# Kernel tuning notes

Hardware: AMD Instinct MI355X
Metric: run time of the kernel (lower is better)

Reference implementation:

```python
import jax, jax.numpy as jnp
import numpy as np

B, S, HID = 2, 2048, 2048
NH, NKV, HD = 16, 4, 128
GROUPS = NH // NKV
CLIP = 8.0
ROPE_THETA = 500000.0
QKV_OUT = HID + 2 * NKV * HD  # 3072
NEG = jnp.finfo(jnp.float32).min


def setup_inputs() -> dict:
    key = jax.random.key(0)
    k1, k2, k3 = jax.random.split(key, 3)
    hidden_states = jax.random.normal(k1, (B, S, HID), dtype=jnp.float32)
    position_ids = jnp.tile(jnp.arange(S, dtype=jnp.int64)[None, :], (B, 1))
    Wqkv = jax.random.normal(k2, (QKV_OUT, HID), dtype=jnp.float32) * (HID ** -0.5)
    Wout = jax.random.normal(k3, (HID, HID), dtype=jnp.float32) * (HID ** -0.5)
    return {"hidden_states": hidden_states, "position_ids": position_ids,
            "Wqkv": Wqkv, "Wout": Wout}


def _rotate_half(x):
    x1, x2 = jnp.split(x, 2, axis=-1)
    return jnp.concatenate((-x2, x1), axis=-1)


def reference(hidden_states, position_ids, Wqkv, Wout):
    b, s, _ = hidden_states.shape
    # fused QKV projection + clamp
    qkv = jnp.einsum('bsh,oh->bso', hidden_states, Wqkv)
    qkv = jnp.clip(qkv, -CLIP, CLIP)
    q, k, v = jnp.split(qkv, [HID, HID + NKV * HD], axis=2)
    q = q.reshape(b, s, NH, HD).transpose(0, 2, 1, 3)   # [b, nh, s, hd]
    k = k.reshape(b, s, NKV, HD).transpose(0, 2, 1, 3)  # [b, nkv, s, hd]
    v = v.reshape(b, s, NKV, HD).transpose(0, 2, 1, 3)
    # rotary embedding
    inv_freq = 1.0 / (ROPE_THETA ** (jnp.arange(0, HD, 2, dtype=jnp.float32) / HD))
    freqs = position_ids.astype(jnp.float32)[:, :, None] * inv_freq[None, None, :]  # [b,s,hd/2]
    emb = jnp.concatenate((freqs, freqs), axis=-1)      # [b, s, hd]
    cos = jnp.cos(emb)[:, None, :, :]                   # [b, 1, s, hd]
    sin = jnp.sin(emb)[:, None, :, :]
    q = q * cos + _rotate_half(q) * sin
    k = k * cos + _rotate_half(k) * sin
    # repeat kv heads (GQA)
    k = jnp.repeat(k, GROUPS, axis=1)  # [b, nh, s, hd]
    v = jnp.repeat(v, GROUPS, axis=1)
    # attention with additive causal mask
    scores = jnp.einsum('bhqd,bhkd->bhqk', q, k) / jnp.sqrt(jnp.float32(HD))
    causal = jnp.where(jnp.tril(jnp.ones((s, s), dtype=bool)), 0.0, NEG)
    scores = scores + causal[None, None, :, :]
    attn = jax.nn.softmax(scores.astype(jnp.float32), axis=-1).astype(q.dtype)
    out = jnp.einsum('bhqk,bhkd->bhqd', attn, v)
    out = out.transpose(0, 2, 1, 3).reshape(b, s, HID)
    return jnp.einsum('bsh,oh->bso', out, Wout)
```

## Files before the change

kernel.cpp:

```cpp
#include <hip/hip_runtime.h>
#include <stdint.h>

#define S_    2048
#define HID_  2048
#define NH_   16
#define NKV_  4
#define HD_   128

using short4x = __attribute__((ext_vector_type(4))) short;
using short8  = __attribute__((ext_vector_type(8))) short;
using floatx4 = __attribute__((ext_vector_type(4))) float;

#define NEGBIG (-3.0e38f)

__device__ __forceinline__ unsigned short f2bf(float x) {
  union { float f; unsigned u; } v; v.f = x;
  unsigned r = v.u + 0x7fffu + ((v.u >> 16) & 1u);
  return (unsigned short)(r >> 16);
}
__device__ __forceinline__ float bf2f(unsigned short b) {
  union { unsigned u; float f; } v; v.u = ((unsigned)b) << 16;
  return v.f;
}
__device__ __forceinline__ void ld_lds16(const void* g, void* l) {
  __builtin_amdgcn_global_load_lds(
      (const __attribute__((address_space(1))) unsigned*)g,
      (__attribute__((address_space(3))) unsigned*)l, 16, 0, 0);
}

__global__ void k_cvt3(const float* __restrict__ s0, unsigned short* __restrict__ d0, int n0,
                       const float* __restrict__ s1, unsigned short* __restrict__ d1, int n1,
                       const float* __restrict__ s2, unsigned short* __restrict__ d2, int n2) {
  int i = blockIdx.x * blockDim.x + threadIdx.x;
  const float* s; unsigned short* d;
  if (i < n0) { s = s0; d = d0; }
  else if (i < n0 + n1) { s = s1; d = d1; i -= n0; }
  else { s = s2; d = d2; i -= n0 + n1; if (i >= n2) return; }
  float4 v = ((const float4*)s)[i];
  union { unsigned short us[4]; uint2 u2; } u;
  u.us[0] = f2bf(v.x); u.us[1] = f2bf(v.y); u.us[2] = f2bf(v.z); u.us[3] = f2bf(v.w);
  ((uint2*)d)[i] = u.u2;
}

__global__ void k_rope2(unsigned short* __restrict__ Qb, unsigned short* __restrict__ Kb,
                        const int* __restrict__ pos, int nQ, float qscale) {
  int idx = blockIdx.x * blockDim.x + threadIdx.x;
  unsigned short* buf; int nh; float oscale;
  if (idx < nQ) { buf = Qb; nh = NH_; oscale = qscale; }
  else { buf = Kb; nh = NKV_; oscale = 1.0f; idx -= nQ; }
  int d = idx & 63;
  int h = (idx >> 6) % nh;
  int m = idx / (unsigned)(nh << 6);
  float p = (float)pos[m];
  float inv = expf(-(float)d * (13.122363377404328f / 64.0f));
  float f = p * inv;
  float cs = cosf(f), sn = sinf(f);
  size_t base = (size_t)m * (nh * HD_) + h * HD_ + d;
  float x1 = bf2f(buf[base]), x2 = bf2f(buf[base + 64]);
  buf[base]      = f2bf((x1 * cs - x2 * sn) * oscale);
  buf[base + 64] = f2bf((x2 * cs + x1 * sn) * oscale);
}

template <int EPI>
__global__ void __launch_bounds__(256)
k_gemm_bt(const unsigned short* __restrict__ A, const unsigned short* __restrict__ Bw,
          unsigned short* __restrict__ Qb, unsigned short* __restrict__ Kb,
          unsigned short* __restrict__ Vt, float* __restrict__ Of) {
  const int K = HID_;
  __shared__ __align__(16) unsigned short As[128 * 32];
  __shared__ __align__(16) unsigned short Bs[128 * 32];
  const int tid  = threadIdx.x;
  const int wave = tid >> 6, lane = tid & 63;
  const int quad = lane >> 4, l15 = lane & 15;
  const int wm = (wave >> 1) * 64, wn = (wave & 1) * 64;
  const int m0 = blockIdx.x * 128, n0 = blockIdx.y * 128;

  floatx4 acc[4][4] = {};

  const int srow = tid >> 2;
  const int scol = (tid & 3) * 8;
  const unsigned short* Ag0 = A  + (size_t)(m0 + srow)      * K + scol;
  const unsigned short* Ag1 = A  + (size_t)(m0 + 64 + srow) * K + scol;
  const unsigned short* Bg0 = Bw + (size_t)(n0 + srow)      * K + scol;
  const unsigned short* Bg1 = Bw + (size_t)(n0 + 64 + srow) * K + scol;
  unsigned short* lA0 = &As[tid * 8];
  unsigned short* lA1 = &As[2048 + tid * 8];
  unsigned short* lB0 = &Bs[tid * 8];
  unsigned short* lB1 = &Bs[2048 + tid * 8];

  for (int k0 = 0; k0 < K; k0 += 32) {
    __syncthreads();
    ld_lds16(Ag0 + k0, lA0);
    ld_lds16(Ag1 + k0, lA1);
    ld_lds16(Bg0 + k0, lB0);
    ld_lds16(Bg1 + k0, lB1);
    __syncthreads();
    short8 a[4], b[4];
#pragma unroll
    for (int i = 0; i < 4; i++) a[i] = *(const short8*)&As[(wm + i * 16 + l15) * 32 + quad * 8];
#pragma unroll
    for (int j = 0; j < 4; j++) b[j] = *(const short8*)&Bs[(wn + j * 16 + l15) * 32 + quad * 8];
#pragma unroll
    for (int i = 0; i < 4; i++)
#pragma unroll
      for (int j = 0; j < 4; j++)
        acc[i][j] = __builtin_amdgcn_mfma_f32_16x16x32_bf16(a[i], b[j], acc[i][j], 0, 0, 0);
  }

#pragma unroll
  for (int i = 0; i < 4; i++) {
#pragma unroll
    for (int j = 0; j < 4; j++) {
      const int col = n0 + wn + j * 16 + l15;
#pragma unroll
      for (int r = 0; r < 4; r++) {
        const int row = m0 + wm + i * 16 + quad * 4 + r;
        float x = acc[i][j][r];
        if (EPI == 0) {
          x = fminf(fmaxf(x, -8.0f), 8.0f);
          if (col < HID_) {
            Qb[(size_t)row * HID_ + col] = f2bf(x);
          } else if (col < HID_ + NKV_ * HD_) {
            Kb[(size_t)row * (NKV_ * HD_) + (col - HID_)] = f2bf(x);
          } else {
            int oo = col - (HID_ + NKV_ * HD_);
            int kvh = oo >> 7, d = oo & 127;
            int bb = row >> 11, ss = row & 2047;
            Vt[((size_t)((bb * NKV_ + kvh) * HD_ + d) << 11) + ss] = f2bf(x);
          }
        } else {
          Of[(size_t)row * HID_ + col] = x;
        }
      }
    }
  }
}

__global__ void __launch_bounds__(256, 2)
k_attn(const unsigned short* __restrict__ Qb, const unsigned short* __restrict__ Kb,
       const unsigned short* __restrict__ Vt, unsigned short* __restrict__ AO) {
  __shared__ __align__(16) unsigned short sm[2][16384];
  __shared__ __align__(16) unsigned short Pl[4][16][80];

  const int tid  = threadIdx.x;
  const int wave = tid >> 6, lane = tid & 63;
  const int quad = lane >> 4, l15 = lane & 15;
  const int tLow  = blockIdx.x;
  const int tHigh = 31 - tLow;
  const int q0L = tLow * 64, q0H = tHigh * 64;
  const int bh = blockIdx.y;
  const int b = bh >> 4, h = bh & 15;
  const int kvh = h >> 2;

  const int srow = tid >> 2;
  const int scol = (tid & 3) * 8;

  {
    const unsigned short* qgL = Qb + (size_t)(b * S_ + q0L + srow) * HID_ + h * HD_ + scol;
    const unsigned short* qgH = Qb + (size_t)(b * S_ + q0H + srow) * HID_ + h * HD_ + scol;
#pragma unroll
    for (int i = 0; i < 4; i++) ld_lds16(qgL + i * 32, &sm[0][i * 2048 + tid * 8]);
#pragma unroll
    for (int i = 0; i < 4; i++) ld_lds16(qgH + i * 32, &sm[1][i * 2048 + tid * 8]);
  }
  __syncthreads();
  short8 qaL[4], qaH[4];
#pragma unroll
  for (int c = 0; c < 4; c++) {
    qaL[c] = *(const short8*)&sm[0][(c * 64 + wave * 16 + l15) * 32 + quad * 8];
    qaH[c] = *(const short8*)&sm[1][(c * 64 + wave * 16 + l15) * 32 + quad * 8];
  }
  __syncthreads();

  floatx4 oacL[8] = {}, oacH[8] = {};
  floatx4 oacEL = {}, oacEH = {};
  float mL = NEGBIG, mH = NEGBIG;

  const unsigned short* kgb = Kb + (size_t)b * S_ * (NKV_ * HD_) + kvh * HD_ + scol;
  const unsigned short* vgb = Vt + (size_t)(b * NKV_ + kvh) * HD_ * S_;

  unsigned short* PlW = &Pl[wave][0][0];

  short8 ones;
#pragma unroll
  for (int i = 0; i < 8; i++) ones[i] = (short)0x3F80;

  auto stage = [&](int bufI, int j) {
    unsigned short* B = &sm[bufI][0];
    const unsigned short* kg = kgb + (size_t)(j * 64 + srow) * (NKV_ * HD_);
#pragma unroll
    for (int i = 0; i < 4; i++) ld_lds16(kg + i * 32, &B[i * 2048 + tid * 8]);
#pragma unroll
    for (int i = 0; i < 4; i++) {
      int c = i >> 1, rowd = (i & 1) * 64 + srow;
      ld_lds16(vgb + (size_t)rowd * S_ + j * 64 + c * 32 + scol,
               &B[8192 + c * 4096 + (i & 1) * 2048 + tid * 8]);
    }
  };

  auto softmax_tile = [&](floatx4* sc, floatx4* oac, floatx4& oacE, float& m_run,
                          int q0, int j, bool diag, short8& pa0, short8& pa1) {
    if (diag) {
      const int rowq = q0 + wave * 16 + l15;
#pragma unroll
      for (int t = 0; t < 4; t++) {
        const int kb0 = j * 64 + t * 16 + quad * 4;
#pragma unroll
        for (int r = 0; r < 4; r++)
          if (kb0 + r > rowq) sc[t][r] = NEGBIG;
      }
    }
    float mx = sc[0][0];
#pragma unroll
    for (int t = 0; t < 4; t++)
#pragma unroll
      for (int r = 0; r < 4; r++) mx = fmaxf(mx, sc[t][r]);
    mx = fmaxf(mx, __shfl_xor(mx, 16));
    mx = fmaxf(mx, __shfl_xor(mx, 32));

    const float mo = m_run;
    m_run = fmaxf(mo, mx);
    if (__any(mx > mo)) {
      float alpha = __builtin_amdgcn_exp2f(mo - m_run);
      float al4[4];
#pragma unroll
      for (int r = 0; r < 4; r++) al4[r] = __shfl(alpha, quad * 4 + r, 16);
#pragma unroll
      for (int t = 0; t < 8; t++)
#pragma unroll
        for (int r = 0; r < 4; r++) oac[t][r] *= al4[r];
#pragma unroll
      for (int r = 0; r < 4; r++) oacE[r] *= al4[r];
    }
#pragma unroll
    for (int t = 0; t < 4; t++) {
      short4x pk;
#pragma unroll
      for (int r = 0; r < 4; r++)
        pk[r] = (short)f2bf(__builtin_amdgcn_exp2f(sc[t][r] - m_run));
      *(short4x*)&PlW[l15 * 80 + t * 16 + quad * 4] = pk;
    }
    pa0 = *(const short8*)&PlW[l15 * 80 + quad * 8];
    pa1 = *(const short8*)&PlW[l15 * 80 + 32 + quad * 8];
  };

  auto step_two = [&](int j, const unsigned short* Kt, const unsigned short* Vts,
                      bool diagL, bool diagH) {
    floatx4 scH[4] = {}, scL[4] = {};
#pragma unroll
    for (int t = 0; t < 4; t++)
#pragma unroll
      for (int c = 0; c < 4; c++) {
        short8 ka = *(const short8*)&Kt[c * 2048 + (t * 16 + l15) * 32 + quad * 8];
        scH[t] = __builtin_amdgcn_mfma_f32_16x16x32_bf16(ka, qaH[c], scH[t], 0, 0, 0);
        scL[t] = __builtin_amdgcn_mfma_f32_16x16x32_bf16(ka, qaL[c], scL[t], 0, 0, 0);
      }
    short8 paH0, paH1, paL0, paL1;
    softmax_tile(scH, oacH, oacEH, mH, q0H, j, diagH, paH0, paH1);
    softmax_tile(scL, oacL, oacEL, mL, q0L, j, diagL, paL0, paL1);
#pragma unroll
    for (int t = 0; t < 8; t++) {
      short8 vb0 = *(const short8*)&Vts[(t * 16 + l15) * 32 + quad * 8];
      oacH[t] = __builtin_amdgcn_mfma_f32_16x16x32_bf16(paH0, vb0, oacH[t], 0, 0, 0);
      oacL[t] = __builtin_amdgcn_mfma_f32_16x16x32_bf16(paL0, vb0, oacL[t], 0, 0, 0);
      short8 vb1 = *(const short8*)&Vts[4096 + (t * 16 + l15) * 32 + quad * 8];
      oacH[t] = __builtin_amdgcn_mfma_f32_16x16x32_bf16(paH1, vb1, oacH[t], 0, 0, 0);
      oacL[t] = __builtin_amdgcn_mfma_f32_16x16x32_bf16(paL1, vb1, oacL[t], 0, 0, 0);
    }
    oacEH = __builtin_amdgcn_mfma_f32_16x16x32_bf16(paH0, ones, oacEH, 0, 0, 0);
    oacEH = __builtin_amdgcn_mfma_f32_16x16x32_bf16(paH1, ones, oacEH, 0, 0, 0);
    oacEL = __builtin_amdgcn_mfma_f32_16x16x32_bf16(paL0, ones, oacEL, 0, 0, 0);
    oacEL = __builtin_amdgcn_mfma_f32_16x16x32_bf16(paL1, ones, oacEL, 0, 0, 0);
  };

  auto step_one = [&](int j, const unsigned short* Kt, const unsigned short* Vts, bool diagH) {
    floatx4 scH[4] = {};
#pragma unroll
    for (int t = 0; t < 4; t++)
#pragma unroll
      for (int c = 0; c < 4; c++) {
        short8 ka = *(const short8*)&Kt[c * 2048 + (t * 16 + l15) * 32 + quad * 8];
        scH[t] = __builtin_amdgcn_mfma_f32_16x16x32_bf16(ka, qaH[c], scH[t], 0, 0, 0);
      }
    short8 paH0, paH1;
    softmax_tile(scH, oacH, oacEH, mH, q0H, j, diagH, paH0, paH1);
#pragma unroll
    for (int t = 0; t < 8; t++) {
      short8 vb0 = *(const short8*)&Vts[(t * 16 + l15) * 32 + quad * 8];
      oacH[t] = __builtin_amdgcn_mfma_f32_16x16x32_bf16(paH0, vb0, oacH[t], 0, 0, 0);
      short8 vb1 = *(const short8*)&Vts[4096 + (t * 16 + l15) * 32 + quad * 8];
      oacH[t] = __builtin_amdgcn_mfma_f32_16x16x32_bf16(paH1, vb1, oacH[t], 0, 0, 0);
    }
    oacEH = __builtin_amdgcn_mfma_f32_16x16x32_bf16(paH0, ones, oacEH, 0, 0, 0);
    oacEH = __builtin_amdgcn_mfma_f32_16x16x32_bf16(paH1, ones, oacEH, 0, 0, 0);
  };

  stage(0, 0);
  int cur = 0;
  for (int j = 0; j <= tHigh; ++j) {
    __syncthreads();
    if (j < tHigh) stage(cur ^ 1, j + 1);
    const unsigned short* Kt  = &sm[cur][0];
    const unsigned short* Vts = Kt + 8192;
    if (j <= tLow) step_two(j, Kt, Vts, j == tLow, j == tHigh);
    else           step_one(j, Kt, Vts, j == tHigh);
    cur ^= 1;
  }

#pragma unroll
  for (int t = 0; t < 8; t++)
#pragma unroll
    for (int r = 0; r < 4; r++) {
      int rgL = q0L + wave * 16 + quad * 4 + r;
      int rgH = q0H + wave * 16 + quad * 4 + r;
      AO[(size_t)(b * S_ + rgL) * HID_ + h * HD_ + t * 16 + l15] = f2bf(oacL[t][r] / oacEL[r]);
      AO[(size_t)(b * S_ + rgH) * HID_ + h * HD_ + t * 16 + l15] = f2bf(oacH[t][r] / oacEH[r]);
    }
}

extern "C" void kernel_launch(void* const* d_in, const int* in_sizes, int n_in,
                              void* d_out, int out_size, void* d_ws, size_t ws_size,
                              hipStream_t stream) {
  (void)in_sizes; (void)n_in; (void)out_size; (void)ws_size;
  const float* hidden = (const float*)d_in[0];
  const int*   pos    = (const int*)d_in[1];
  const float* Wqkv   = (const float*)d_in[2];
  const float* Wout   = (const float*)d_in[3];
  float* out = (float*)d_out;

  unsigned short* ws = (unsigned short*)d_ws;
  const size_t M1 = 1024 * 1024;
  unsigned short* hb  = ws;
  unsigned short* wqb = ws + 8 * M1;
  unsigned short* wob = ws + 14 * M1;
  unsigned short* Qb  = ws + 18 * M1;
  unsigned short* Kb  = ws + 26 * M1;
  unsigned short* Vt  = ws + 28 * M1;
  unsigned short* AO  = hb;

  const float QSCL = 0.08838834764831845f * 1.4426950408889634f;
  const int nQrope = 2 * 2048 * NH_ * 64;
  const int nKrope = 2 * 2048 * NKV_ * 64;

  k_cvt3<<<18432, 256, 0, stream>>>(hidden, hb, 2097152,
                                    Wqkv, wqb, 1572864,
                                    Wout, wob, 1048576);
  k_gemm_bt<0><<<dim3(32, 24), 256, 0, stream>>>(hb, wqb, Qb, Kb, Vt, nullptr);
  k_rope2<<<(nQrope + nKrope) / 256, 256, 0, stream>>>(Qb, Kb, pos, nQrope, QSCL);
  k_attn<<<dim3(16, 32), 256, 0, stream>>>(Qb, Kb, Vt, AO);
  k_gemm_bt<1><<<dim3(32, 16), 256, 0, stream>>>(AO, wob, nullptr, nullptr, nullptr, out);
}
```

Measured before the change: 319.6 us.

## Use hardware bf16 pack, deepen GEMM k-step, and swizzle block order

Replaces software round-to-nearest bf16 conversion with the v_cvt_pk_bf16_f32 instruction, packing pairs in the convert kernel and in the attention softmax P writes. The GEMM now stages 64 k-elements per barrier pair instead of 32, halving the synchronisation count at the cost of doubled LDS use. Blocks are remapped from a 2D grid to a 1D grouped order of four N-tiles per column band to improve L2 reuse of the weight and activation tiles. The hardware conversion may differ slightly in NaN/rounding edge cases.

```diff
diff --git a/kernel.cpp b/kernel.cpp
--- a/kernel.cpp
+++ b/kernel.cpp
@@ -7,16 +7,18 @@
 #define NKV_  4
 #define HD_   128
 
-using short4x = __attribute__((ext_vector_type(4))) short;
 using short8  = __attribute__((ext_vector_type(8))) short;
 using floatx4 = __attribute__((ext_vector_type(4))) float;
 
 #define NEGBIG (-3.0e38f)
 
+__device__ __forceinline__ unsigned pkbf(float a, float b) {
+  unsigned r;
+  asm("v_cvt_pk_bf16_f32 %0, %1, %2" : "=v"(r) : "v"(a), "v"(b));
+  return r;
+}
 __device__ __forceinline__ unsigned short f2bf(float x) {
-  union { float f; unsigned u; } v; v.f = x;
-  unsigned r = v.u + 0x7fffu + ((v.u >> 16) & 1u);
-  return (unsigned short)(r >> 16);
+  return (unsigned short)(pkbf(x, 0.f) & 0xffffu);
 }
 __device__ __forceinline__ float bf2f(unsigned short b) {
   union { unsigned u; float f; } v; v.u = ((unsigned)b) << 16;
@@ -37,9 +39,8 @@
   else if (i < n0 + n1) { s = s1; d = d1; i -= n0; }
   else { s = s2; d = d2; i -= n0 + n1; if (i >= n2) return; }
   float4 v = ((const float4*)s)[i];
-  union { unsigned short us[4]; uint2 u2; } u;
-  u.us[0] = f2bf(v.x); u.us[1] = f2bf(v.y); u.us[2] = f2bf(v.z); u.us[3] = f2bf(v.w);
-  ((uint2*)d)[i] = u.u2;
+  uint2 u; u.x = pkbf(v.x, v.y); u.y = pkbf(v.z, v.w);
+  ((uint2*)d)[i] = u;
 }
 
 __global__ void k_rope2(unsigned short* __restrict__ Qb, unsigned short* __restrict__ Kb,
@@ -65,46 +66,51 @@
 __global__ void __launch_bounds__(256)
 k_gemm_bt(const unsigned short* __restrict__ A, const unsigned short* __restrict__ Bw,
           unsigned short* __restrict__ Qb, unsigned short* __restrict__ Kb,
-          unsigned short* __restrict__ Vt, float* __restrict__ Of) {
+          unsigned short* __restrict__ Vt, float* __restrict__ Of, int Mt) {
   const int K = HID_;
-  __shared__ __align__(16) unsigned short As[128 * 32];
-  __shared__ __align__(16) unsigned short Bs[128 * 32];
+  __shared__ __align__(16) unsigned short As[2][4096];
+  __shared__ __align__(16) unsigned short Bs[2][4096];
   const int tid  = threadIdx.x;
   const int wave = tid >> 6, lane = tid & 63;
   const int quad = lane >> 4, l15 = lane & 15;
   const int wm = (wave >> 1) * 64, wn = (wave & 1) * 64;
-  const int m0 = blockIdx.x * 128, n0 = blockIdx.y * 128;
+
+  const int bid = blockIdx.x;
+  const int sc4 = bid / (Mt * 4);
+  const int rr  = bid % (Mt * 4);
+  const int m0 = (rr % Mt) * 128;
+  const int n0 = (sc4 * 4 + rr / Mt) * 128;
 
   floatx4 acc[4][4] = {};
 
   const int srow = tid >> 2;
   const int scol = (tid & 3) * 8;
-  const unsigned short* Ag0 = A  + (size_t)(m0 + srow)      * K + scol;
-  const unsigned short* Ag1 = A  + (size_t)(m0 + 64 + srow) * K + scol;
-  const unsigned short* Bg0 = Bw + (size_t)(n0 + srow)      * K + scol;
-  const unsigned short* Bg1 = Bw + (size_t)(n0 + 64 + srow) * K + scol;
-  unsigned short* lA0 = &As[tid * 8];
-  unsigned short* lA1 = &As[2048 + tid * 8];
-  unsigned short* lB0 = &Bs[tid * 8];
-  unsigned short* lB1 = &Bs[2048 + tid * 8];
-
-  for (int k0 = 0; k0 < K; k0 += 32) {
+  const unsigned short* Ag = A  + (size_t)(m0 + srow) * K + scol;
+  const unsigned short* Bg = Bw + (size_t)(n0 + srow) * K + scol;
+
+  for (int k0 = 0; k0 < K; k0 += 64) {
     __syncthreads();
-    ld_lds16(Ag0 + k0, lA0);
-    ld_lds16(Ag1 + k0, lA1);
-    ld_lds16(Bg0 + k0, lB0);
-    ld_lds16(Bg1 + k0, lB1);
+#pragma unroll
+    for (int c = 0; c < 2; c++)
+#pragma unroll
+      for (int rb = 0; rb < 2; rb++) {
+        ld_lds16(Ag + (size_t)(rb * 64) * K + k0 + c * 32, &As[c][rb * 2048 + tid * 8]);
+        ld_lds16(Bg + (size_t)(rb * 64) * K + k0 + c * 32, &Bs[c][rb * 2048 + tid * 8]);
+      }
     __syncthreads();
-    short8 a[4], b[4];
-#pragma unroll
-    for (int i = 0; i < 4; i++) a[i] = *(const short8*)&As[(wm + i * 16 + l15) * 32 + quad * 8];
-#pragma unroll
-    for (int j = 0; j < 4; j++) b[j] = *(const short8*)&Bs[(wn + j * 16 + l15) * 32 + quad * 8];
-#pragma unroll
-    for (int i = 0; i < 4; i++)
-#pragma unroll
-      for (int j = 0; j < 4; j++)
-        acc[i][j] = __builtin_amdgcn_mfma_f32_16x16x32_bf16(a[i], b[j], acc[i][j], 0, 0, 0);
+#pragma unroll
+    for (int h = 0; h < 2; h++) {
+      short8 a[4], b[4];
+#pragma unroll
+      for (int i = 0; i < 4; i++) a[i] = *(const short8*)&As[h][(wm + i * 16 + l15) * 32 + quad * 8];
+#pragma unroll
+      for (int j = 0; j < 4; j++) b[j] = *(const short8*)&Bs[h][(wn + j * 16 + l15) * 32 + quad * 8];
+#pragma unroll
+      for (int i = 0; i < 4; i++)
+#pragma unroll
+        for (int j = 0; j < 4; j++)
+          acc[i][j] = __builtin_amdgcn_mfma_f32_16x16x32_bf16(a[i], b[j], acc[i][j], 0, 0, 0);
+    }
   }
 
 #pragma unroll
@@ -234,11 +240,12 @@
     }
 #pragma unroll
     for (int t = 0; t < 4; t++) {
-      short4x pk;
-#pragma unroll
-      for (int r = 0; r < 4; r++)
-        pk[r] = (short)f2bf(__builtin_amdgcn_exp2f(sc[t][r] - m_run));
-      *(short4x*)&PlW[l15 * 80 + t * 16 + quad * 4] = pk;
+      float p0 = __builtin_amdgcn_exp2f(sc[t][0] - m_run);
+      float p1 = __builtin_amdgcn_exp2f(sc[t][1] - m_run);
+      float p2 = __builtin_amdgcn_exp2f(sc[t][2] - m_run);
+      float p3 = __builtin_amdgcn_exp2f(sc[t][3] - m_run);
+      uint2 pk; pk.x = pkbf(p0, p1); pk.y = pkbf(p2, p3);
+      *(uint2*)&PlW[l15 * 80 + t * 16 + quad * 4] = pk;
     }
     pa0 = *(const short8*)&PlW[l15 * 80 + quad * 8];
     pa1 = *(const short8*)&PlW[l15 * 80 + 32 + quad * 8];
@@ -345,8 +352,8 @@
   k_cvt3<<<18432, 256, 0, stream>>>(hidden, hb, 2097152,
                                     Wqkv, wqb, 1572864,
                                     Wout, wob, 1048576);
-  k_gemm_bt<0><<<dim3(32, 24), 256, 0, stream>>>(hb, wqb, Qb, Kb, Vt, nullptr);
+  k_gemm_bt<0><<<768, 256, 0, stream>>>(hb, wqb, Qb, Kb, Vt, nullptr, 32);
   k_rope2<<<(nQrope + nKrope) / 256, 256, 0, stream>>>(Qb, Kb, pos, nQrope, QSCL);
   k_attn<<<dim3(16, 32), 256, 0, stream>>>(Qb, Kb, Vt, AO);
-  k_gemm_bt<1><<<dim3(32, 16), 256, 0, stream>>>(AO, wob, nullptr, nullptr, nullptr, out);
-}
+  k_gemm_bt<1><<<512, 256, 0, stream>>>(AO, wob, nullptr, nullptr, nullptr, out, 32);
+}
```

Result: slower. 329.4 us (+3.0%).
